# Performance work log

Hardware: AMD Instinct MI355X
Metric: run time of the kernel (lower is better)

The kernel has to match this reference:

```python
import jax, jax.numpy as jnp
import numpy as np

N, K, D = 65536, 1024, 512
INIT_COUNT = 100


def setup_inputs() -> dict:
    key = jax.random.key(0)
    k1, k2 = jax.random.split(key)
    embedded = jax.random.normal(k1, (N, D), dtype=jnp.float32)
    centers = jax.random.normal(k2, (K, D), dtype=jnp.float32)
    count = jnp.full((K,), INIT_COUNT, dtype=jnp.int32)  # start_training: ones(K)*100
    return {"embedded": embedded, "centers": centers, "count": count}


def reference(embedded, centers, count):
    # --- squared_euclidean_distance(centers, embedded): dist[n,k] = ||e_n - c_k||^2 ---
    e2 = jnp.sum(embedded * embedded, axis=-1, keepdims=True)   # [N,1]
    c2 = jnp.sum(centers * centers, axis=-1)                    # [K]
    cross = embedded @ centers.T                                # [N,K] GEMM
    dist = e2 + c2[None, :] - 2.0 * cross                       # [N,K]

    # compression_loss: min over clusters, then mean
    loss = jnp.mean(jnp.min(dist, axis=1))

    # prediction_hard: hard assignments
    s = jnp.argmin(dist, axis=1)                                # [N] int

    # update_centroids: the per-sample EMA with eta = 1/count[c] is exactly an
    # incremental (running) mean seeded with `count` pseudo-counts, so the
    # sequential loop is mathematically equivalent to a vectorized segment mean:
    #   new_centers[c] = (count[c]*centers[c] + sum_{s_i=c} e_i) / (count[c] + n_c)
    added = jax.ops.segment_sum(embedded, s, num_segments=K)                       # [K,D]
    n_add = jax.ops.segment_sum(jnp.ones_like(s, dtype=jnp.int32), s, num_segments=K)  # [K]
    new_count = count + n_add
    cf = count.astype(centers.dtype)[:, None]
    new_centers = (cf * centers + added) / new_count.astype(centers.dtype)[:, None]

    return loss, s, new_centers, new_count
```

## Files before the change

kernel.cpp:

```cpp
#include <hip/hip_runtime.h>

#define N_SAMPLES 65536
#define K_CENT    1024
#define DIM       512
#define TAU 0.125f

typedef __attribute__((ext_vector_type(8))) short  short8;
typedef _Float16 half8 __attribute__((ext_vector_type(8)));
typedef __attribute__((ext_vector_type(4))) float  float4v;

__device__ inline unsigned short f2h_bits(float x) {
    _Float16 h = (_Float16)x;
    return __builtin_bit_cast(unsigned short, h);
}

__global__ __launch_bounds__(256) void hsplit_c2_kernel(const float* __restrict__ cen,
                                                        unsigned short* __restrict__ Bh,
                                                        float* __restrict__ c2) {
    const int k = blockIdx.x, t = threadIdx.x;
    const float* row = cen + (size_t)k * DIM;
    float2 v = ((const float2*)row)[t];
    unsigned int packed = (unsigned)f2h_bits(v.x) | ((unsigned)f2h_bits(v.y) << 16);
    *(unsigned int*)(Bh + (size_t)k * DIM + t * 2) = packed;
    float s = v.x * v.x + v.y * v.y;
    for (int off = 32; off; off >>= 1) s += __shfl_down(s, off);
    __shared__ float w4[4];
    int lane = t & 63, wv = t >> 6;
    if (lane == 0) w4[wv] = s;
    __syncthreads();
    if (t == 0) c2[k] = w4[0] + w4[1] + w4[2] + w4[3];
}

__global__ __launch_bounds__(256, 4) void assign_mfma(
    const float* __restrict__ A,
    const unsigned short* __restrict__ Bh,
    const float* __restrict__ c2,
    float* __restrict__ pbest,
    float* __restrict__ psec,
    int* __restrict__ pidx)
{
    __shared__ __align__(16) unsigned short Bt[4096];
    __shared__ float st_best[128];
    __shared__ float st_sec[128];
    __shared__ int   st_idx[128];

    const int tid  = threadIdx.x;
    const int w    = tid >> 6;
    const int lane = tid & 63;
    const int quad = lane >> 4;
    const int l15  = lane & 15;
    const int mblk  = blockIdx.x & 511;
    const int chunk = blockIdx.x >> 9;
    const int m0   = mblk * 128;

    if (tid < 128) { st_best[tid] = 3.4e38f; st_sec[tid] = 3.4e38f; st_idx[tid] = 0; }

    const float* aBase = A + (size_t)(m0 + w * 32 + l15) * DIM + quad * 8;

    for (int nt = 0; nt < 4; ++nt) {
        const int n0 = chunk * 512 + nt * 128;
        float4v acc[16];
        #pragma unroll
        for (int z = 0; z < 16; ++z) acc[z] = (float4v){0.f, 0.f, 0.f, 0.f};

        for (int ks = 0; ks < 16; ++ks) {
            float4 av[2][2];
            #pragma unroll
            for (int i = 0; i < 2; ++i) {
                const float* ap = aBase + i * 16 * DIM + ks * 32;
                av[i][0] = *(const float4*)ap;
                av[i][1] = *(const float4*)(ap + 4);
            }

            __syncthreads();
            #pragma unroll
            for (int i = 0; i < 2; ++i) {
                int s = i * 256 + tid;
                int qq = s >> 7, r = s & 127;
                *(short8*)&Bt[s * 8] =
                    *(const short8*)(Bh + (size_t)(n0 + r) * DIM + ks * 32 + qq * 8);
            }
            __syncthreads();

            half8 ah[2], al[2];
            #pragma unroll
            for (int i = 0; i < 2; ++i) {
                float f[8] = {av[i][0].x, av[i][0].y, av[i][0].z, av[i][0].w,
                              av[i][1].x, av[i][1].y, av[i][1].z, av[i][1].w};
                #pragma unroll
                for (int e = 0; e < 8; ++e) {
                    _Float16 h = (_Float16)f[e];
                    ah[i][e] = h;
                    al[i][e] = (_Float16)(f[e] - (float)h);
                }
            }

            #pragma unroll
            for (int j4 = 0; j4 < 8; ++j4) {
                short8 braw = *(const short8*)&Bt[(quad * 128 + j4 * 16 + l15) * 8];
                half8 bh = __builtin_bit_cast(half8, braw);
                #pragma unroll
                for (int i = 0; i < 2; ++i) {
                    acc[i * 8 + j4] = __builtin_amdgcn_mfma_f32_16x16x32_f16(
                        ah[i], bh, acc[i * 8 + j4], 0, 0, 0);
                    acc[i * 8 + j4] = __builtin_amdgcn_mfma_f32_16x16x32_f16(
                        al[i], bh, acc[i * 8 + j4], 0, 0, 0);
                }
            }
        }

        float c2v[8];
        #pragma unroll
        for (int j = 0; j < 8; ++j) c2v[j] = c2[n0 + j * 16 + l15];
        #pragma unroll
        for (int i = 0; i < 2; ++i)
            #pragma unroll
            for (int reg = 0; reg < 4; ++reg) {
                float bv = 3.4e38f, sv = 3.4e38f; int bi = 0;
                #pragma unroll
                for (int j = 0; j < 8; ++j) {
                    float v = c2v[j] - 2.0f * acc[i * 8 + j][reg];
                    int n = n0 + j * 16 + l15;
                    if (v < bv) { sv = bv; bv = v; bi = n; }
                    else if (v < sv) sv = v;
                }
                #pragma unroll
                for (int mask = 1; mask < 16; mask <<= 1) {
                    float ob = __shfl_xor(bv, mask);
                    float os = __shfl_xor(sv, mask);
                    int   oi = __shfl_xor(bi, mask);
                    float ns = fminf(fminf(sv, os), fmaxf(bv, ob));
                    if (ob < bv || (ob == bv && oi < bi)) { bv = ob; bi = oi; }
                    sv = ns;
                }
                if (l15 == 0) {
                    int ml = w * 32 + i * 16 + quad * 4 + reg;
                    float sb = st_best[ml], ss = st_sec[ml]; int si = st_idx[ml];
                    float ns = fminf(fminf(ss, sv), fmaxf(sb, bv));
                    if (bv < sb || (bv == sb && bi < si)) { st_best[ml] = bv; st_idx[ml] = bi; }
                    st_sec[ml] = ns;
                }
            }
    }

    __syncthreads();
    if (tid < 128) {
        int m = m0 + tid;
        pbest[chunk * N_SAMPLES + m] = st_best[tid];
        psec [chunk * N_SAMPLES + m] = st_sec[tid];
        pidx [chunk * N_SAMPLES + m] = st_idx[tid];
    }
}

__global__ __launch_bounds__(256) void merge_kernel(
    const float* __restrict__ pbest,
    const float* __restrict__ psec,
    const int* __restrict__ pidx,
    int* __restrict__ s_idx,
    float* __restrict__ out_s,
    int* __restrict__ hist,
    int* __restrict__ flag_cnt,
    int* __restrict__ flagged,
    float* __restrict__ out_loss)
{
    int m = blockIdx.x * 256 + threadIdx.x;
    float b0 = pbest[m], b1 = pbest[N_SAMPLES + m];
    float s0 = psec[m],  s1 = psec[N_SAMPLES + m];
    int   i0 = pidx[m],  i1 = pidx[N_SAMPLES + m];
    float bv, sv; int bi;
    if (b1 < b0) { bv = b1; bi = i1; sv = fminf(b0, s1); }
    else         { bv = b0; bi = i0; sv = fminf(s0, b1); }
    s_idx[m] = bi;
    out_s[m] = (float)bi;
    atomicAdd(&hist[bi], 1);
    if (sv - bv < TAU) { int p = atomicAdd(flag_cnt, 1); flagged[p] = m; }

    float ls = bv;
    for (int off = 32; off; off >>= 1) ls += __shfl_down(ls, off);
    __shared__ float ws4[4];
    int lane = threadIdx.x & 63, wv = threadIdx.x >> 6;
    if (lane == 0) ws4[wv] = ls;
    __syncthreads();
    if (threadIdx.x == 0)
        atomicAdd(out_loss, (ws4[0] + ws4[1] + ws4[2] + ws4[3]) * (1.0f / N_SAMPLES));
}

__global__ __launch_bounds__(256) void refine_kernel(
    const float* __restrict__ emb,
    const float* __restrict__ cen,
    const int* __restrict__ flag_cnt,
    const int* __restrict__ flagged,
    int* __restrict__ s_idx,
    float* __restrict__ out_s,
    int* __restrict__ hist)
{
    __shared__ float e_sh[DIM];
    __shared__ double rvd[256];
    __shared__ int rid[256];
    const int t = threadIdx.x;
    const int cnt = *flag_cnt;
    for (int idx = blockIdx.x; idx < cnt; idx += gridDim.x) {
        int n = flagged[idx];
        __syncthreads();
        ((float2*)e_sh)[t] = ((const float2*)(emb + (size_t)n * DIM))[t];
        __syncthreads();
        double bestd = 1e300;
        int bestk = 0;
        #pragma unroll
        for (int j = 0; j < 4; ++j) {
            int k = t * 4 + j;
            const float* crow = cen + (size_t)k * DIM;
            double acc = 0.0;
            for (int d = 0; d < DIM; d += 4) {
                float4 cv = *(const float4*)(crow + d);
                double d0 = (double)e_sh[d + 0] - (double)cv.x;
                double d1 = (double)e_sh[d + 1] - (double)cv.y;
                double d2 = (double)e_sh[d + 2] - (double)cv.z;
                double d3 = (double)e_sh[d + 3] - (double)cv.w;
                acc += d0 * d0 + d1 * d1 + d2 * d2 + d3 * d3;
            }
            if (acc < bestd) { bestd = acc; bestk = k; }
        }
        rvd[t] = bestd; rid[t] = bestk;
        __syncthreads();
        for (int off = 128; off; off >>= 1) {
            if (t < off) {
                double v = rvd[t + off]; int ii = rid[t + off];
                if (v < rvd[t] || (v == rvd[t] && ii < rid[t])) { rvd[t] = v; rid[t] = ii; }
            }
            __syncthreads();
        }
        if (t == 0) {
            int old = s_idx[n], nw = rid[0];
            if (nw != old) {
                atomicSub(&hist[old], 1);
                atomicAdd(&hist[nw], 1);
                s_idx[n] = nw;
                out_s[n] = (float)nw;
            }
        }
    }
}

__global__ void scan_kernel(const int* __restrict__ hist,
                            int* __restrict__ offsets,
                            int* __restrict__ cursor,
                            const int* __restrict__ count_in,
                            float* __restrict__ out_count) {
    __shared__ int sbuf[K_CENT];
    int t = threadIdx.x;
    int v = hist[t];
    sbuf[t] = v;
    __syncthreads();
    for (int off = 1; off < K_CENT; off <<= 1) {
        int x = (t >= off) ? sbuf[t - off] : 0;
        __syncthreads();
        sbuf[t] += x;
        __syncthreads();
    }
    int incl = sbuf[t];
    offsets[t] = incl - v;
    cursor[t]  = incl - v;
    out_count[t] = (float)(count_in[t] + v);
    if (t == K_CENT - 1) offsets[K_CENT] = incl;
}

__global__ void scatter_kernel(const int* __restrict__ s_idx,
                               int* __restrict__ cursor,
                               int* __restrict__ order) {
    int n = blockIdx.x * blockDim.x + threadIdx.x;
    if (n < N_SAMPLES) {
        int pos = atomicAdd(&cursor[s_idx[n]], 1);
        order[pos] = n;
    }
}

__global__ __launch_bounds__(256) void gp_kernel(
    const float* __restrict__ emb,
    const int* __restrict__ s_idx,
    const int* __restrict__ order,
    float* __restrict__ accum,
    float* __restrict__ out_loss)
{
    __shared__ int s_n[64], s_c[64];
    const int t = threadIdx.x;
    const int base = blockIdx.x * 64;
    if (t < 64) { int n = order[base + t]; s_n[t] = n; s_c[t] = s_idx[n]; }
    __syncthreads();
    float ax = 0.f, ay = 0.f, ssq = 0.f;
    int cur = s_c[0];
    for (int r = 0; r < 64; ++r) {
        int n = s_n[r], c = s_c[r];
        if (c != cur) {
            atomicAdd(&accum[(size_t)cur * DIM + t * 2], ax);
            atomicAdd(&accum[(size_t)cur * DIM + t * 2 + 1], ay);
            ax = ay = 0.f; cur = c;
        }
        float2 e = *(const float2*)(emb + (size_t)n * DIM + t * 2);
        ax += e.x; ay += e.y;
        ssq += e.x * e.x + e.y * e.y;
    }
    atomicAdd(&accum[(size_t)cur * DIM + t * 2], ax);
    atomicAdd(&accum[(size_t)cur * DIM + t * 2 + 1], ay);

    for (int off = 32; off; off >>= 1) ssq += __shfl_down(ssq, off);
    __shared__ float wsum[4];
    if ((t & 63) == 0) wsum[t >> 6] = ssq;
    __syncthreads();
    if (t == 0)
        atomicAdd(out_loss, (wsum[0] + wsum[1] + wsum[2] + wsum[3]) * (1.0f / N_SAMPLES));
}

__global__ __launch_bounds__(256) void combine_kernel(
    const float* __restrict__ centers,
    const int* __restrict__ count_in,
    const int* __restrict__ hist,
    const float* __restrict__ accum,
    float* __restrict__ out_centers)
{
    int k = blockIdx.x, t = threadIdx.x;
    float cn = (float)count_in[k];
    float tot = cn + (float)hist[k];
    float2 c = *(const float2*)(centers + (size_t)k * DIM + t * 2);
    float2 a = *(const float2*)(accum   + (size_t)k * DIM + t * 2);
    float2 o;
    o.x = (cn * c.x + a.x) / tot;
    o.y = (cn * c.y + a.y) / tot;
    *(float2*)(out_centers + (size_t)k * DIM + t * 2) = o;
}

extern "C" void kernel_launch(void* const* d_in, const int* in_sizes, int n_in,
                              void* d_out, int out_size, void* d_ws, size_t ws_size,
                              hipStream_t stream) {
    const float* emb = (const float*)d_in[0];
    const float* cen = (const float*)d_in[1];
    const int*   cnt = (const int*)d_in[2];

    float* out = (float*)d_out;
    float* out_loss    = out;
    float* out_s       = out + 1;
    float* out_centers = out + 1 + N_SAMPLES;
    float* out_count   = out + 1 + N_SAMPLES + (size_t)K_CENT * DIM;

    int* wsi = (int*)d_ws;
    int*   hist     = wsi;
    int*   offsets  = wsi + 1024;
    int*   cursor   = wsi + 2064;
    int*   s_idx    = wsi + 4096;
    float* c2       = (float*)(wsi + 69632);
    int*   flag_cnt = wsi + 70656;
    int*   flagged  = wsi + 70720;
    float* pbest    = (float*)(wsi + 136256);
    float* psec     = (float*)(wsi + 267328);
    int*   pidx     = wsi + 398400;
    unsigned short* Bh = (unsigned short*)(wsi + 529472);
    int*   order    = wsi + 136256;
    float* accum    = (float*)(wsi + 529472);

    hipMemsetAsync(hist, 0, K_CENT * sizeof(int), stream);
    hipMemsetAsync(out_loss, 0, sizeof(float), stream);
    hipMemsetAsync(flag_cnt, 0, sizeof(int), stream);

    hsplit_c2_kernel<<<K_CENT, 256, 0, stream>>>(cen, Bh, c2);
    assign_mfma<<<1024, 256, 0, stream>>>(emb, Bh, c2, pbest, psec, pidx);
    merge_kernel<<<N_SAMPLES / 256, 256, 0, stream>>>(pbest, psec, pidx, s_idx, out_s,
                                                      hist, flag_cnt, flagged, out_loss);
    hipMemsetAsync(accum, 0, (size_t)K_CENT * DIM * sizeof(float), stream);
    refine_kernel<<<256, 256, 0, stream>>>(emb, cen, flag_cnt, flagged, s_idx, out_s, hist);
    scan_kernel<<<1, K_CENT, 0, stream>>>(hist, offsets, cursor, cnt, out_count);
    scatter_kernel<<<N_SAMPLES / 256, 256, 0, stream>>>(s_idx, cursor, order);
    gp_kernel<<<N_SAMPLES / 64, 256, 0, stream>>>(emb, s_idx, order, accum, out_loss);
    combine_kernel<<<K_CENT, 256, 0, stream>>>(cen, cnt, hist, accum, out_centers);
}
```

Measured before the change: 679.7 us.

## Double-buffer B tiles via direct global-to-LDS loads and prefetch A registers

Doubles the LDS buffer for B. The next k-slice of the fp16 centroid tile is now fetched with global_load_lds straight into the alternate buffer, instead of going through registers behind two barriers. The fp32 A operand for the next k-step is loaded into registers while the current MFMAs run, and split to hi/lo fp16 only after them. This cuts one barrier per k-step and overlaps global latency with compute. The cost is double the B LDS footprint and more live registers, which may affect occupancy at launch bounds of 4 blocks.

```diff
diff --git a/kernel.cpp b/kernel.cpp
--- a/kernel.cpp
+++ b/kernel.cpp
@@ -13,6 +13,11 @@
     _Float16 h = (_Float16)x;
     return __builtin_bit_cast(unsigned short, h);
 }
+
+#define GLD16(gsrc, ldst)                                                        \
+    __builtin_amdgcn_global_load_lds(                                            \
+        (const __attribute__((address_space(1))) unsigned int*)(gsrc),           \
+        (__attribute__((address_space(3))) unsigned int*)(ldst), 16, 0, 0)
 
 __global__ __launch_bounds__(256) void hsplit_c2_kernel(const float* __restrict__ cen,
                                                         unsigned short* __restrict__ Bh,
@@ -31,6 +36,29 @@
     if (t == 0) c2[k] = w4[0] + w4[1] + w4[2] + w4[3];
 }
 
+__device__ inline void loadA(const float* aBase, int kc, float4 av[2][2]) {
+    #pragma unroll
+    for (int i = 0; i < 2; ++i) {
+        const float* ap = aBase + i * 16 * DIM + kc;
+        av[i][0] = *(const float4*)ap;
+        av[i][1] = *(const float4*)(ap + 4);
+    }
+}
+
+__device__ inline void cvtA(const float4 av[2][2], half8 ah[2], half8 al[2]) {
+    #pragma unroll
+    for (int i = 0; i < 2; ++i) {
+        float f[8] = {av[i][0].x, av[i][0].y, av[i][0].z, av[i][0].w,
+                      av[i][1].x, av[i][1].y, av[i][1].z, av[i][1].w};
+        #pragma unroll
+        for (int e = 0; e < 8; ++e) {
+            _Float16 h = (_Float16)f[e];
+            ah[i][e] = h;
+            al[i][e] = (_Float16)(f[e] - (float)h);
+        }
+    }
+}
+
 __global__ __launch_bounds__(256, 4) void assign_mfma(
     const float* __restrict__ A,
     const unsigned short* __restrict__ Bh,
@@ -39,7 +67,7 @@
     float* __restrict__ psec,
     int* __restrict__ pidx)
 {
-    __shared__ __align__(16) unsigned short Bt[4096];
+    __shared__ __align__(16) unsigned short Bt[2][4096];
     __shared__ float st_best[128];
     __shared__ float st_sec[128];
     __shared__ int   st_idx[128];
@@ -57,56 +85,48 @@
 
     const float* aBase = A + (size_t)(m0 + w * 32 + l15) * DIM + quad * 8;
 
+    const int s0 = tid, s1 = 256 + tid;
+    const unsigned short* bsrc0 = Bh + (size_t)(s0 & 127) * DIM + ((s0 >> 7) * 8);
+    const unsigned short* bsrc1 = Bh + (size_t)(s1 & 127) * DIM + ((s1 >> 7) * 8);
+
     for (int nt = 0; nt < 4; ++nt) {
         const int n0 = chunk * 512 + nt * 128;
+        const size_t nOff = (size_t)n0 * DIM;
         float4v acc[16];
         #pragma unroll
         for (int z = 0; z < 16; ++z) acc[z] = (float4v){0.f, 0.f, 0.f, 0.f};
 
+        GLD16(bsrc0 + nOff, &Bt[0][s0 * 8]);
+        GLD16(bsrc1 + nOff, &Bt[0][s1 * 8]);
+        float4 avN[2][2];
+        half8 ahC[2], alC[2];
+        loadA(aBase, 0, avN);
+        cvtA(avN, ahC, alC);
+
         for (int ks = 0; ks < 16; ++ks) {
-            float4 av[2][2];
-            #pragma unroll
-            for (int i = 0; i < 2; ++i) {
-                const float* ap = aBase + i * 16 * DIM + ks * 32;
-                av[i][0] = *(const float4*)ap;
-                av[i][1] = *(const float4*)(ap + 4);
-            }
-
             __syncthreads();
-            #pragma unroll
-            for (int i = 0; i < 2; ++i) {
-                int s = i * 256 + tid;
-                int qq = s >> 7, r = s & 127;
-                *(short8*)&Bt[s * 8] =
-                    *(const short8*)(Bh + (size_t)(n0 + r) * DIM + ks * 32 + qq * 8);
-            }
-            __syncthreads();
-
-            half8 ah[2], al[2];
-            #pragma unroll
-            for (int i = 0; i < 2; ++i) {
-                float f[8] = {av[i][0].x, av[i][0].y, av[i][0].z, av[i][0].w,
-                              av[i][1].x, av[i][1].y, av[i][1].z, av[i][1].w};
-                #pragma unroll
-                for (int e = 0; e < 8; ++e) {
-                    _Float16 h = (_Float16)f[e];
-                    ah[i][e] = h;
-                    al[i][e] = (_Float16)(f[e] - (float)h);
-                }
-            }
-
+            if (ks < 15) {
+                const int kc = (ks + 1) * 32;
+                GLD16(bsrc0 + nOff + kc, &Bt[(ks + 1) & 1][s0 * 8]);
+                GLD16(bsrc1 + nOff + kc, &Bt[(ks + 1) & 1][s1 * 8]);
+                loadA(aBase, kc, avN);
+            }
+
+            const unsigned short* bb = Bt[ks & 1];
             #pragma unroll
             for (int j4 = 0; j4 < 8; ++j4) {
-                short8 braw = *(const short8*)&Bt[(quad * 128 + j4 * 16 + l15) * 8];
+                short8 braw = *(const short8*)&bb[(quad * 128 + j4 * 16 + l15) * 8];
                 half8 bh = __builtin_bit_cast(half8, braw);
                 #pragma unroll
                 for (int i = 0; i < 2; ++i) {
                     acc[i * 8 + j4] = __builtin_amdgcn_mfma_f32_16x16x32_f16(
-                        ah[i], bh, acc[i * 8 + j4], 0, 0, 0);
+                        ahC[i], bh, acc[i * 8 + j4], 0, 0, 0);
                     acc[i * 8 + j4] = __builtin_amdgcn_mfma_f32_16x16x32_f16(
-                        al[i], bh, acc[i * 8 + j4], 0, 0, 0);
+                        alC[i], bh, acc[i * 8 + j4], 0, 0, 0);
                 }
             }
+
+            if (ks < 15) cvtA(avN, ahC, alC);
         }
 
         float c2v[8];
```

Result: faster. 661.2 us (-2.7%).

## Pre-pack centers into MFMA fragment layout and drop LDS staging in assign GEMM

Applied to the files above, without the earlier changes.

The center matrix is now packed once into a layout that matches the MFMA B-fragment order. Each wave then loads its B operands directly from global memory (coalesced, one short8 per lane) instead of staging them through LDS with two __syncthreads per k-step. The A tile for the next k-step is software-prefetched while the current MFMAs run. Loss accumulation moves to a double atomic that is finalized in combine_kernel. Direct global B loads rely on L2/L1 reuse across blocks and waves, and may add memory traffic compared with shared staging.

```diff
diff --git a/kernel.cpp b/kernel.cpp
--- a/kernel.cpp
+++ b/kernel.cpp
@@ -14,32 +14,58 @@
     return __builtin_bit_cast(unsigned short, h);
 }
 
-__global__ __launch_bounds__(256) void hsplit_c2_kernel(const float* __restrict__ cen,
-                                                        unsigned short* __restrict__ Bh,
-                                                        float* __restrict__ c2) {
-    const int k = blockIdx.x, t = threadIdx.x;
-    const float* row = cen + (size_t)k * DIM;
-    float2 v = ((const float2*)row)[t];
-    unsigned int packed = (unsigned)f2h_bits(v.x) | ((unsigned)f2h_bits(v.y) << 16);
-    *(unsigned int*)(Bh + (size_t)k * DIM + t * 2) = packed;
-    float s = v.x * v.x + v.y * v.y;
+__global__ __launch_bounds__(256) void pack_kernel(const float* __restrict__ cen,
+                                                   unsigned short* __restrict__ Bp,
+                                                   float* __restrict__ c2) {
+    const int wv = threadIdx.x >> 6, lane = threadIdx.x & 63;
+    const int k = blockIdx.x * 4 + wv;
+    const int kk = lane >> 2, quad = lane & 3;
+    const float* src = cen + (size_t)k * DIM + kk * 32 + quad * 8;
+    float4 v0 = *(const float4*)src;
+    float4 v1 = *(const float4*)(src + 4);
+    float f[8] = {v0.x, v0.y, v0.z, v0.w, v1.x, v1.y, v1.z, v1.w};
+    short8 h;
+    float s = 0.f;
+    #pragma unroll
+    for (int e = 0; e < 8; ++e) { h[e] = (short)f2h_bits(f[e]); s += f[e] * f[e]; }
+    const int ntG = k >> 7, j4 = (k >> 4) & 7, l15 = k & 15;
+    size_t slot = (size_t)(ntG * 16 + kk) * 512 + j4 * 64 + quad * 16 + l15;
+    *(short8*)(Bp + slot * 8) = h;
     for (int off = 32; off; off >>= 1) s += __shfl_down(s, off);
-    __shared__ float w4[4];
-    int lane = t & 63, wv = t >> 6;
-    if (lane == 0) w4[wv] = s;
-    __syncthreads();
-    if (t == 0) c2[k] = w4[0] + w4[1] + w4[2] + w4[3];
+    if (lane == 0) c2[k] = s;
+}
+
+__device__ inline void loadA(const float* aBase, int kc, float4 av[2][2]) {
+    #pragma unroll
+    for (int i = 0; i < 2; ++i) {
+        const float* ap = aBase + (size_t)i * 16 * DIM + kc;
+        av[i][0] = *(const float4*)ap;
+        av[i][1] = *(const float4*)(ap + 4);
+    }
+}
+
+__device__ inline void cvtA(const float4 av[2][2], half8 ah[2], half8 al[2]) {
+    #pragma unroll
+    for (int i = 0; i < 2; ++i) {
+        float f[8] = {av[i][0].x, av[i][0].y, av[i][0].z, av[i][0].w,
+                      av[i][1].x, av[i][1].y, av[i][1].z, av[i][1].w};
+        #pragma unroll
+        for (int e = 0; e < 8; ++e) {
+            _Float16 h = (_Float16)f[e];
+            ah[i][e] = h;
+            al[i][e] = (_Float16)(f[e] - (float)h);
+        }
+    }
 }
 
 __global__ __launch_bounds__(256, 4) void assign_mfma(
     const float* __restrict__ A,
-    const unsigned short* __restrict__ Bh,
+    const unsigned short* __restrict__ Bp,
     const float* __restrict__ c2,
     float* __restrict__ pbest,
     float* __restrict__ psec,
     int* __restrict__ pidx)
 {
-    __shared__ __align__(16) unsigned short Bt[4096];
     __shared__ float st_best[128];
     __shared__ float st_sec[128];
     __shared__ int   st_idx[128];
@@ -54,50 +80,37 @@
     const int m0   = mblk * 128;
 
     if (tid < 128) { st_best[tid] = 3.4e38f; st_sec[tid] = 3.4e38f; st_idx[tid] = 0; }
+    __syncthreads();
 
     const float* aBase = A + (size_t)(m0 + w * 32 + l15) * DIM + quad * 8;
 
     for (int nt = 0; nt < 4; ++nt) {
-        const int n0 = chunk * 512 + nt * 128;
+        const int ntG = chunk * 4 + nt;
+        const int n0  = ntG * 128;
+        const unsigned short* bBase = Bp + (size_t)ntG * 16 * 4096;
+
         float4v acc[16];
         #pragma unroll
         for (int z = 0; z < 16; ++z) acc[z] = (float4v){0.f, 0.f, 0.f, 0.f};
 
+        float4 avN[2][2];
+        half8 ah[2], al[2];
+        loadA(aBase, 0, avN);
+        cvtA(avN, ah, al);
+
         for (int ks = 0; ks < 16; ++ks) {
-            float4 av[2][2];
+            const unsigned short* bk = bBase + (size_t)ks * 4096;
+
+            short8 br0 = *(const short8*)(bk + 0 * 512 + lane * 8);
+            short8 br1 = *(const short8*)(bk + 1 * 512 + lane * 8);
+            short8 br2 = *(const short8*)(bk + 2 * 512 + lane * 8);
+            short8 br3 = *(const short8*)(bk + 3 * 512 + lane * 8);
+
+            if (ks < 15) loadA(aBase, (ks + 1) * 32, avN);
+
             #pragma unroll
-            for (int i = 0; i < 2; ++i) {
-                const float* ap = aBase + i * 16 * DIM + ks * 32;
-                av[i][0] = *(const float4*)ap;
-                av[i][1] = *(const float4*)(ap + 4);
-            }
-
-            __syncthreads();
-            #pragma unroll
-            for (int i = 0; i < 2; ++i) {
-                int s = i * 256 + tid;
-                int qq = s >> 7, r = s & 127;
-                *(short8*)&Bt[s * 8] =
-                    *(const short8*)(Bh + (size_t)(n0 + r) * DIM + ks * 32 + qq * 8);
-            }
-            __syncthreads();
-
-            half8 ah[2], al[2];
-            #pragma unroll
-            for (int i = 0; i < 2; ++i) {
-                float f[8] = {av[i][0].x, av[i][0].y, av[i][0].z, av[i][0].w,
-                              av[i][1].x, av[i][1].y, av[i][1].z, av[i][1].w};
-                #pragma unroll
-                for (int e = 0; e < 8; ++e) {
-                    _Float16 h = (_Float16)f[e];
-                    ah[i][e] = h;
-                    al[i][e] = (_Float16)(f[e] - (float)h);
-                }
-            }
-
-            #pragma unroll
-            for (int j4 = 0; j4 < 8; ++j4) {
-                short8 braw = *(const short8*)&Bt[(quad * 128 + j4 * 16 + l15) * 8];
+            for (int j4 = 0; j4 < 4; ++j4) {
+                short8 braw = (j4 == 0) ? br0 : (j4 == 1) ? br1 : (j4 == 2) ? br2 : br3;
                 half8 bh = __builtin_bit_cast(half8, braw);
                 #pragma unroll
                 for (int i = 0; i < 2; ++i) {
@@ -107,6 +120,25 @@
                         al[i], bh, acc[i * 8 + j4], 0, 0, 0);
                 }
             }
+
+            short8 br4 = *(const short8*)(bk + 4 * 512 + lane * 8);
+            short8 br5 = *(const short8*)(bk + 5 * 512 + lane * 8);
+            short8 br6 = *(const short8*)(bk + 6 * 512 + lane * 8);
+            short8 br7 = *(const short8*)(bk + 7 * 512 + lane * 8);
+            #pragma unroll
+            for (int j4 = 4; j4 < 8; ++j4) {
+                short8 braw = (j4 == 4) ? br4 : (j4 == 5) ? br5 : (j4 == 6) ? br6 : br7;
+                half8 bh = __builtin_bit_cast(half8, braw);
+                #pragma unroll
+                for (int i = 0; i < 2; ++i) {
+                    acc[i * 8 + j4] = __builtin_amdgcn_mfma_f32_16x16x32_f16(
+                        ah[i], bh, acc[i * 8 + j4], 0, 0, 0);
+                    acc[i * 8 + j4] = __builtin_amdgcn_mfma_f32_16x16x32_f16(
+                        al[i], bh, acc[i * 8 + j4], 0, 0, 0);
+                }
+            }
+
+            if (ks < 15) cvtA(avN, ah, al);
         }
 
         float c2v[8];
@@ -161,7 +193,7 @@
     int* __restrict__ hist,
     int* __restrict__ flag_cnt,
     int* __restrict__ flagged,
-    float* __restrict__ out_loss)
+    double* __restrict__ loss_d)
 {
     int m = blockIdx.x * 256 + threadIdx.x;
     float b0 = pbest[m], b1 = pbest[N_SAMPLES + m];
@@ -182,7 +214,7 @@
     if (lane == 0) ws4[wv] = ls;
     __syncthreads();
     if (threadIdx.x == 0)
-        atomicAdd(out_loss, (ws4[0] + ws4[1] + ws4[2] + ws4[3]) * (1.0f / N_SAMPLES));
+        atomicAdd(loss_d, (double)(ws4[0] + ws4[1] + ws4[2] + ws4[3]));
 }
 
 __global__ __launch_bounds__(256) void refine_kernel(
@@ -280,7 +312,7 @@
     const int* __restrict__ s_idx,
     const int* __restrict__ order,
     float* __restrict__ accum,
-    float* __restrict__ out_loss)
+    double* __restrict__ loss_d)
 {
     __shared__ int s_n[64], s_c[64];
     const int t = threadIdx.x;
@@ -308,7 +340,7 @@
     if ((t & 63) == 0) wsum[t >> 6] = ssq;
     __syncthreads();
     if (t == 0)
-        atomicAdd(out_loss, (wsum[0] + wsum[1] + wsum[2] + wsum[3]) * (1.0f / N_SAMPLES));
+        atomicAdd(loss_d, (double)(wsum[0] + wsum[1] + wsum[2] + wsum[3]));
 }
 
 __global__ __launch_bounds__(256) void combine_kernel(
@@ -316,9 +348,12 @@
     const int* __restrict__ count_in,
     const int* __restrict__ hist,
     const float* __restrict__ accum,
-    float* __restrict__ out_centers)
+    const double* __restrict__ loss_d,
+    float* __restrict__ out_centers,
+    float* __restrict__ out_loss)
 {
     int k = blockIdx.x, t = threadIdx.x;
+    if (k == 0 && t == 0) *out_loss = (float)(*loss_d * (1.0 / N_SAMPLES));
     float cn = (float)count_in[k];
     float tot = cn + (float)hist[k];
     float2 c = *(const float2*)(centers + (size_t)k * DIM + t * 2);
@@ -349,26 +384,28 @@
     int*   s_idx    = wsi + 4096;
     float* c2       = (float*)(wsi + 69632);
     int*   flag_cnt = wsi + 70656;
+    double* loss_d  = (double*)(wsi + 70712);
     int*   flagged  = wsi + 70720;
     float* pbest    = (float*)(wsi + 136256);
     float* psec     = (float*)(wsi + 267328);
     int*   pidx     = wsi + 398400;
-    unsigned short* Bh = (unsigned short*)(wsi + 529472);
+    unsigned short* Bp = (unsigned short*)(wsi + 529472);
     int*   order    = wsi + 136256;
     float* accum    = (float*)(wsi + 529472);
 
     hipMemsetAsync(hist, 0, K_CENT * sizeof(int), stream);
-    hipMemsetAsync(out_loss, 0, sizeof(float), stream);
+    hipMemsetAsync(loss_d, 0, sizeof(double), stream);
     hipMemsetAsync(flag_cnt, 0, sizeof(int), stream);
 
-    hsplit_c2_kernel<<<K_CENT, 256, 0, stream>>>(cen, Bh, c2);
-    assign_mfma<<<1024, 256, 0, stream>>>(emb, Bh, c2, pbest, psec, pidx);
+    pack_kernel<<<256, 256, 0, stream>>>(cen, Bp, c2);
+    assign_mfma<<<1024, 256, 0, stream>>>(emb, Bp, c2, pbest, psec, pidx);
     merge_kernel<<<N_SAMPLES / 256, 256, 0, stream>>>(pbest, psec, pidx, s_idx, out_s,
-                                                      hist, flag_cnt, flagged, out_loss);
+                                                      hist, flag_cnt, flagged, loss_d);
     hipMemsetAsync(accum, 0, (size_t)K_CENT * DIM * sizeof(float), stream);
     refine_kernel<<<256, 256, 0, stream>>>(emb, cen, flag_cnt, flagged, s_idx, out_s, hist);
     scan_kernel<<<1, K_CENT, 0, stream>>>(hist, offsets, cursor, cnt, out_count);
     scatter_kernel<<<N_SAMPLES / 256, 256, 0, stream>>>(s_idx, cursor, order);
-    gp_kernel<<<N_SAMPLES / 64, 256, 0, stream>>>(emb, s_idx, order, accum, out_loss);
-    combine_kernel<<<K_CENT, 256, 0, stream>>>(cen, cnt, hist, accum, out_centers);
-}
+    gp_kernel<<<N_SAMPLES / 64, 256, 0, stream>>>(emb, s_idx, order, accum, loss_d);
+    combine_kernel<<<K_CENT, 256, 0, stream>>>(cen, cnt, hist, accum, loss_d,
+                                               out_centers, out_loss);
+}
```

Result: faster. 652.2 us (-4.0%).
